# Kernel optimization log

Measured on AMD Instinct MI355X. Metric: run time of the kernel, lower is better.

## Reference

```python
import jax, jax.numpy as jnp
import numpy as np

N_USERS, N_ITEMS, N_TOPICS = 200000, 100000, 100
N_NODES = N_USERS + N_ITEMS + N_TOPICS
N_EDGES = 5000000
DIM = 64
LAYERS = 3
BATCH = 16384


def setup_inputs() -> dict:
    key = jax.random.key(0)
    ks = jax.random.split(key, 8)
    users = jax.random.randint(ks[0], (BATCH,), 0, N_USERS, dtype=jnp.int64 if jax.config.jax_enable_x64 else jnp.int32)
    items = jax.random.randint(ks[1], (BATCH,), 0, N_ITEMS, dtype=jnp.int64 if jax.config.jax_enable_x64 else jnp.int32)
    edge_rows = jax.random.randint(ks[2], (N_EDGES,), 0, N_NODES, dtype=jnp.int32)
    edge_cols = jax.random.randint(ks[3], (N_EDGES,), 0, N_NODES, dtype=jnp.int32)
    # values ~ 1/deg to mimic the symmetric-normalized A_hat of LightGCN
    edge_vals = jax.random.uniform(ks[4], (N_EDGES,), dtype=jnp.float32) / 16.0
    user_emb = 0.1 * jax.random.normal(ks[5], (N_USERS, DIM), dtype=jnp.float32)
    item_emb = 0.1 * jax.random.normal(ks[6], (N_ITEMS, DIM), dtype=jnp.float32)
    topic_emb = 0.1 * jax.random.normal(ks[7], (N_TOPICS, DIM), dtype=jnp.float32)
    return {"users": users, "items": items, "edge_rows": edge_rows,
            "edge_cols": edge_cols, "edge_vals": edge_vals,
            "user_emb": user_emb, "item_emb": item_emb, "topic_emb": topic_emb}


def reference(users, items, edge_rows, edge_cols, edge_vals, user_emb, item_emb, topic_emb):
    n_users = user_emb.shape[0]
    n_nodes = n_users + item_emb.shape[0] + topic_emb.shape[0]
    # E^0 = [users; items; topics]
    h = jnp.concatenate([user_emb, item_emb, topic_emb], axis=0)  # [N, dim]
    acc = h
    for _ in range(LAYERS):
        # sparse A_hat @ h : gather source rows, scale by edge weight, scatter-add to dst
        msgs = edge_vals[:, None] * h[edge_cols]                  # [E, dim]
        h = jax.ops.segment_sum(msgs, edge_rows, num_segments=n_nodes)
        acc = acc + h
    out = acc / (LAYERS + 1)                                      # stack-mean over layers
    u = out[users]                                                # [B, dim]
    it = out[n_users + items]                                     # items offset into node table
    return jnp.sum(u * it, axis=1)                                # [B]
```

## Files before the change

### kernel.cpp

```cpp
#include <hip/hip_runtime.h>
#include <hip/hip_fp16.h>

#define N_USERS  200000
#define N_ITEMS  100000
#define N_TOPICS 100
#define N_NODES  (N_USERS + N_ITEMS + N_TOPICS)
#define DIM      64
#define BSHIFT   10
#define BROWS    (1 << BSHIFT)
#define NBUCKETS ((N_NODES + BROWS - 1) >> BSHIFT)
#define COLMASK  0x7FFFF
#define NB       512
#define NBSHIFT  9
#define M_TOT    (NBUCKETS * NB)
#define SB       256
#define CH       ((M_TOT + SB - 1) / SB)
#define BUCKET_CAP 24576



__global__ void bucket_hist_kernel(const int* __restrict__ rows,
                                   int* __restrict__ partial, int n_edges) {
    __shared__ int h[NBUCKETS];
    for (int i = threadIdx.x; i < NBUCKETS; i += blockDim.x) h[i] = 0;
    __syncthreads();
    int stride = gridDim.x * blockDim.x;
    for (int e = blockIdx.x * blockDim.x + threadIdx.x; e < n_edges; e += stride)
        atomicAdd(&h[((unsigned)rows[e]) >> BSHIFT], 1);
    __syncthreads();
    for (int i = threadIdx.x; i < NBUCKETS; i += blockDim.x)
        partial[blockIdx.x * NBUCKETS + i] = h[i];
}

__device__ __forceinline__ int phys_idx(int L) {
    return (L & (NB - 1)) * NBUCKETS + (L >> NBSHIFT);
}

__global__ void scanB1_kernel(const int* __restrict__ partial,
                              int* __restrict__ psum) {
    __shared__ int s[256];
    int tid = threadIdx.x;
    int c0 = blockIdx.x * CH;
    int c1 = min(M_TOT, c0 + CH);
    int sum = 0;
    for (int L = c0 + tid; L < c1; L += 256) sum += partial[phys_idx(L)];
    s[tid] = sum;
    __syncthreads();
    for (int off = 128; off > 0; off >>= 1) {
        if (tid < off) s[tid] += s[tid + off];
        __syncthreads();
    }
    if (tid == 0) psum[blockIdx.x] = s[0];
}

__global__ void scanB3_kernel(const int* __restrict__ partial,
                              const int* __restrict__ psum,
                              int* __restrict__ offs) {
    __shared__ int s[SB];
    __shared__ int tile[256];
    __shared__ int carry;
    int tid = threadIdx.x;
    s[tid] = (tid < blockIdx.x) ? psum[tid] : 0;
    __syncthreads();
    for (int off = 128; off > 0; off >>= 1) {
        if (tid < off) s[tid] += s[tid + off];
        __syncthreads();
    }
    if (tid == 0) carry = s[0];
    __syncthreads();
    int c0 = blockIdx.x * CH;
    int c1 = min(M_TOT, c0 + CH);
    for (int base = c0; base < c1; base += 256) {
        int L = base + tid;
        int v = (L < c1) ? partial[phys_idx(L)] : 0;
        tile[tid] = v;
        __syncthreads();
        for (int off = 1; off < 256; off <<= 1) {
            int t = (tid >= off) ? tile[tid - off] : 0;
            __syncthreads();
            tile[tid] += t;
            __syncthreads();
        }
        if (L < c1) offs[L] = carry + tile[tid] - v;
        __syncthreads();
        if (tid == 255) carry += tile[255];
        __syncthreads();
    }
}

__global__ void scatter1_kernel(const int* __restrict__ rows,
                                const int* __restrict__ cols,
                                const float* __restrict__ vals,
                                const int* __restrict__ offs,
                                int2* __restrict__ bkt_buf, int n_edges) {
    __shared__ int lpos[NBUCKETS];
    for (int i = threadIdx.x; i < NBUCKETS; i += blockDim.x)
        lpos[i] = offs[i * NB + blockIdx.x];
    __syncthreads();
    int stride = gridDim.x * blockDim.x;
    for (int e = blockIdx.x * blockDim.x + threadIdx.x; e < n_edges; e += stride) {
        int r = rows[e];
        int b = ((unsigned)r) >> BSHIFT;
        int pos = atomicAdd(&lpos[b], 1);
        int2 p;
        p.x = cols[e] | ((r & (BROWS - 1)) << 19);
        p.y = __float_as_int(vals[e]);
        bkt_buf[pos] = p;
    }
}

__device__ __forceinline__ int pad8(int x) { return (x + 7) & ~7; }

__global__ void scatter2_kernel(const int2* __restrict__ bkt_buf,
                                const int* __restrict__ offs,
                                int2* __restrict__ row_span,
                                int2* __restrict__ csr_cv, int n_edges) {
    __shared__ int lcnt[BROWS];
    __shared__ int lptr[BROWS];
    __shared__ int lfill[BROWS];
    __shared__ int s[512];
    int b = blockIdx.x;
    int t = threadIdx.x;
    int e0 = offs[b * NB];
    int e1 = (b == NBUCKETS - 1) ? n_edges : offs[(b + 1) * NB];
    for (int i = t; i < BROWS; i += 512) { lcnt[i] = 0; lfill[i] = 0; }
    __syncthreads();
    for (int e = e0 + t; e < e1; e += blockDim.x)
        atomicAdd(&lcnt[((unsigned)bkt_buf[e].x) >> 19], 1);
    __syncthreads();
    s[t] = pad8(lcnt[2 * t]) + pad8(lcnt[2 * t + 1]);
    __syncthreads();
    for (int off = 1; off < 512; off <<= 1) {
        int v = (t >= off) ? s[t - off] : 0;
        __syncthreads();
        s[t] += v;
        __syncthreads();
    }
    {
        int base = b * BUCKET_CAP + (t ? s[t - 1] : 0);
        int rbase = b << BSHIFT;
        int pe = pad8(lcnt[2 * t]);
        int po = pad8(lcnt[2 * t + 1]);
        int p_even = base;
        int p_odd  = base + pe;
        lptr[2 * t]     = p_even;
        lptr[2 * t + 1] = p_odd;
        if (rbase + 2 * t < N_NODES) {
            int2 sp; sp.x = p_even; sp.y = p_even + pe;
            row_span[rbase + 2 * t] = sp;
        }
        if (rbase + 2 * t + 1 < N_NODES) {
            int2 sp; sp.x = p_odd; sp.y = p_odd + po;
            row_span[rbase + 2 * t + 1] = sp;
        }
    }
    __syncthreads();
    for (int e = e0 + t; e < e1; e += blockDim.x) {
        int2 p = bkt_buf[e];
        int delta = ((unsigned)p.x) >> 19;
        int pos = lptr[delta] + atomicAdd(&lfill[delta], 1);
        int2 cv;
        cv.x = p.x & COLMASK;
        cv.y = p.y;
        csr_cv[pos] = cv;
    }
    __syncthreads();
    for (int i = t; i < BROWS; i += 512) {
        int c  = lcnt[i];
        int cp = pad8(c);
        int p  = lptr[i];
        int2 z; z.x = 0; z.y = 0;
        for (int k = c; k < cp; ++k) csr_cv[p + k] = z;
    }
}

__global__ void concat_f16_kernel(const float* __restrict__ uemb,
                                  const float* __restrict__ iemb,
                                  const float* __restrict__ temb,
                                  ushort* __restrict__ h0) {
    int g = blockIdx.x * blockDim.x + threadIdx.x;
    long base = (long)g * 4;
    if (base >= (long)N_NODES * DIM) return;
    const float* src;
    long off;
    if (base < (long)N_USERS * DIM)                 { src = uemb; off = base; }
    else if (base < (long)(N_USERS + N_ITEMS) * DIM){ src = iemb; off = base - (long)N_USERS * DIM; }
    else                                            { src = temb; off = base - (long)(N_USERS + N_ITEMS) * DIM; }
    float4 v = *(const float4*)(src + off);
    __half2 a = __floats2half2_rn(v.x, v.y);
    __half2 b = __floats2half2_rn(v.z, v.w);
    uint2 o;
    o.x = *(unsigned*)&a;
    o.y = *(unsigned*)&b;
    ((uint2*)h0)[g] = o;
}

__device__ __forceinline__ float4 fma_mix4(const ushort* __restrict__ h,
                                           int row, int l16, float w,
                                           float4 acc) {
    uint2 r = ((const uint2*)(h + (size_t)row * DIM))[l16];
    __half2 h01 = *(__half2*)&r.x;
    __half2 h23 = *(__half2*)&r.y;
    acc.x = __builtin_fmaf(__half2float(__low2half(h01)),  w, acc.x);
    acc.y = __builtin_fmaf(__half2float(__high2half(h01)), w, acc.y);
    acc.z = __builtin_fmaf(__half2float(__low2half(h23)),  w, acc.z);
    acc.w = __builtin_fmaf(__half2float(__high2half(h23)), w, acc.w);
    return acc;
}

__device__ __forceinline__ float4 batch8(const int2* __restrict__ csr_cv,
                                         const ushort* __restrict__ h_src,
                                         int p, int l16, float4 acc) {
    const int4* q = (const int4*)(csr_cv + p);
    int4 a = q[0], b = q[1], c = q[2], d = q[3];
    acc = fma_mix4(h_src, a.x, l16, __int_as_float(a.y), acc);
    acc = fma_mix4(h_src, a.z, l16, __int_as_float(a.w), acc);
    acc = fma_mix4(h_src, b.x, l16, __int_as_float(b.y), acc);
    acc = fma_mix4(h_src, b.z, l16, __int_as_float(b.w), acc);
    acc = fma_mix4(h_src, c.x, l16, __int_as_float(c.y), acc);
    acc = fma_mix4(h_src, c.z, l16, __int_as_float(c.w), acc);
    acc = fma_mix4(h_src, d.x, l16, __int_as_float(d.y), acc);
    acc = fma_mix4(h_src, d.z, l16, __int_as_float(d.w), acc);
    return acc;
}

__global__ void spmv_csr_kernel(const int2* __restrict__ row_span,
                                const int2* __restrict__ csr_cv,
                                const ushort* __restrict__ h_src,
                                ushort* __restrict__ h_dst) {
    int wave = (int)(((long)blockIdx.x * blockDim.x + threadIdx.x) >> 6);
    int lane = threadIdx.x & 63;
    int g    = lane >> 4;
    int l16  = lane & 15;
    int r    = wave * 4 + g;
    int rc   = min(r, N_NODES - 1);
    int2 sp  = row_span[rc];
    int p0   = sp.x;
    int len  = (r < N_NODES) ? (sp.y - sp.x) : 0;
    int m = max(len, __shfl_xor(len, 16, 64));
    m = max(m, __shfl_xor(m, 32, 64));
    float4 acc = make_float4(0.f, 0.f, 0.f, 0.f);
    for (int off = 0; off < m; off += 8) {
        if (off < len)
            acc = batch8(csr_cv, h_src, p0 + off, l16, acc);
    }
    if (r < N_NODES) {
        __half2 a = __floats2half2_rn(acc.x, acc.y);
        __half2 b = __floats2half2_rn(acc.z, acc.w);
        uint2 o;
        o.x = *(unsigned*)&a;
        o.y = *(unsigned*)&b;
        ((uint2*)(h_dst + (size_t)r * DIM))[l16] = o;
    }
}

__global__ void spmv_batch_kernel(const int2* __restrict__ row_span,
                                  const int2* __restrict__ csr_cv,
                                  const ushort* __restrict__ h_src,
                                  const int* __restrict__ users,
                                  const int* __restrict__ items,
                                  float* __restrict__ u_acc,
                                  float* __restrict__ it_acc, int B) {
    int wave = (int)(((long)blockIdx.x * blockDim.x + threadIdx.x) >> 6);
    int lane = threadIdx.x & 63;
    int g    = lane >> 4;
    int l16  = lane & 15;
    int s    = wave * 4 + g;
    bool ok  = s < 2 * B;
    int node = 0;
    if (ok) node = (s < B) ? users[s] : (N_USERS + items[s - B]);
    int2 sp  = row_span[node];
    int p0   = sp.x;
    int len  = ok ? (sp.y - sp.x) : 0;
    int m = max(len, __shfl_xor(len, 16, 64));
    m = max(m, __shfl_xor(m, 32, 64));
    float4 acc = make_float4(0.f, 0.f, 0.f, 0.f);
    for (int off = 0; off < m; off += 8) {
        if (off < len)
            acc = batch8(csr_cv, h_src, p0 + off, l16, acc);
    }
    if (ok) {
        float* dst = (s < B) ? (u_acc + (size_t)s * DIM)
                             : (it_acc + (size_t)(s - B) * DIM);
        float4* p = (float4*)dst + l16;
        float4 old = *p;
        old.x += acc.x; old.y += acc.y; old.z += acc.z; old.w += acc.w;
        *p = old;
    }
}


__global__ void gather_add_kernel(const ushort* __restrict__ h,
                                  const int* __restrict__ users,
                                  const int* __restrict__ items,
                                  float* __restrict__ u_acc,
                                  float* __restrict__ it_acc,
                                  int B, int first) {
    int gid  = blockIdx.x * blockDim.x + threadIdx.x;
    int b    = gid >> 4;
    int lane = gid & 15;
    if (b >= B) return;
    int u  = users[b];
    int it = N_USERS + items[b];
    uint2 ur = ((const uint2*)(h + (size_t)u  * DIM))[lane];
    uint2 ir = ((const uint2*)(h + (size_t)it * DIM))[lane];
    float2 u01 = __half22float2(*(__half2*)&ur.x);
    float2 u23 = __half22float2(*(__half2*)&ur.y);
    float2 i01 = __half22float2(*(__half2*)&ir.x);
    float2 i23 = __half22float2(*(__half2*)&ir.y);
    float4* up = (float4*)(u_acc  + (size_t)b * DIM) + lane;
    float4* ip = (float4*)(it_acc + (size_t)b * DIM) + lane;
    if (first) {
        *up = make_float4(u01.x, u01.y, u23.x, u23.y);
        *ip = make_float4(i01.x, i01.y, i23.x, i23.y);
    } else {
        float4 a = *up;
        a.x += u01.x; a.y += u01.y; a.z += u23.x; a.w += u23.y;
        *up = a;
        float4 c = *ip;
        c.x += i01.x; c.y += i01.y; c.z += i23.x; c.w += i23.y;
        *ip = c;
    }
}

__global__ void dot_kernel(const float* __restrict__ u_acc,
                           const float* __restrict__ it_acc,
                           float* __restrict__ out, int B) {
    int gid  = blockIdx.x * blockDim.x + threadIdx.x;
    int b    = gid >> 6;
    int lane = gid & 63;
    if (b >= B) return;
    float p = u_acc[(size_t)b * DIM + lane] * it_acc[(size_t)b * DIM + lane];
    #pragma unroll
    for (int off = 32; off > 0; off >>= 1)
        p += __shfl_down(p, off, 64);
    if (lane == 0) out[b] = p * (1.0f / 16.0f);
}

extern "C" void kernel_launch(void* const* d_in, const int* in_sizes, int n_in,
                              void* d_out, int out_size, void* d_ws, size_t ws_size,
                              hipStream_t stream) {
    const int*   users = (const int*)d_in[0];
    const int*   items = (const int*)d_in[1];
    const int*   erows = (const int*)d_in[2];
    const int*   ecols = (const int*)d_in[3];
    const float* evals = (const float*)d_in[4];
    const float* uemb  = (const float*)d_in[5];
    const float* iemb  = (const float*)d_in[6];
    const float* temb  = (const float*)d_in[7];
    float* out = (float*)d_out;

    const int n_edges = in_sizes[2];
    const int B       = in_sizes[0];

    const size_t h2bytes = (((size_t)N_NODES * DIM * 2 + 255) / 256) * 256;
    const size_t abytes  = (size_t)B * DIM * sizeof(float);
    const size_t spbytes = (((size_t)N_NODES * 8 + 255) / 256) * 256;
    const size_t csrbytes= (size_t)NBUCKETS * BUCKET_CAP * 8;
    const size_t bkbytes = (size_t)n_edges * 8;
    const size_t mbytes  = (((size_t)M_TOT * 4 + 255) / 256) * 256;

    char* ws = (char*)d_ws;
    size_t off = 0;
    ushort* hA       = (ushort*)(ws + off); off += h2bytes;
    ushort* hB       = (ushort*)(ws + off); off += h2bytes;
    float*  u_acc    = (float*) (ws + off); off += abytes;
    float*  it_acc   = (float*) (ws + off); off += abytes;
    int2*   row_span = (int2*)  (ws + off); off += spbytes;
    int2*   csr_cv   = (int2*)  (ws + off); off += csrbytes;
    int2*   bkt_buf  = (int2*)  (ws + off); off += bkbytes;
    int*    partial  = (int*)   (ws + off); off += mbytes;
    int*    offs     = (int*)   (ws + off); off += mbytes;
    int*    psum     = (int*)   (ws + off); off += 4096;

    dim3 blk(256);
    dim3 blk512(512);

    bucket_hist_kernel<<<NB, blk512, 0, stream>>>(erows, partial, n_edges);
    scanB1_kernel<<<SB, blk, 0, stream>>>(partial, psum);
    scanB3_kernel<<<SB, blk, 0, stream>>>(partial, psum, offs);
    scatter1_kernel<<<NB, blk512, 0, stream>>>(erows, ecols, evals, offs, bkt_buf, n_edges);
    scatter2_kernel<<<NBUCKETS, blk512, 0, stream>>>(bkt_buf, offs, row_span, csr_cv, n_edges);

    const long n4 = (long)N_NODES * DIM / 4;
    concat_f16_kernel<<<(int)((n4 + 255) / 256), blk, 0, stream>>>(uemb, iemb, temb, hA);

    const int gblocks = (B * 16 + 255) / 256;
    gather_add_kernel<<<gblocks, blk, 0, stream>>>(hA, users, items, u_acc, it_acc, B, 1);

    const int nwaves  = (N_NODES + 3) / 4;
    const int sblocks = (int)(((long)nwaves * 64 + 255) / 256);
    ushort* src = hA;
    ushort* dst = hB;
    for (int l = 0; l < 2; ++l) {
        spmv_csr_kernel<<<sblocks, blk, 0, stream>>>(row_span, csr_cv, src, dst);
        gather_add_kernel<<<gblocks, blk, 0, stream>>>(dst, users, items, u_acc, it_acc, B, 0);
        ushort* t = src; src = dst; dst = t;
    }
    const int bwaves  = (2 * B + 3) / 4;
    const int bblocks = (int)(((long)bwaves * 64 + 255) / 256);
    spmv_batch_kernel<<<bblocks, blk, 0, stream>>>(row_span, csr_cv, src,
                                                   users, items, u_acc, it_acc, B);

    dot_kernel<<<(B * 64 + 255) / 256, blk, 0, stream>>>(u_acc, it_acc, out, B);
}
```

Baseline: 548.5 us.

## Fuse concat into histogram kernel and gather-adds into SpMV launches

Merges the fp16 concat of embeddings into the bucket histogram kernel using extra blocks. Folds each layer's gather-add of batch user/item rows into the SpMV launch that reads that layer's source, and has the final batch SpMV add the previous layer's rows itself. This removes several small kernel launches and their serialization gaps. The trade-off is heterogeneous blocks inside one grid and a larger launch for the prep kernel.

```diff
diff --git a/kernel.cpp b/kernel.cpp
--- a/kernel.cpp
+++ b/kernel.cpp
@@ -19,17 +19,39 @@
 
 
 
-__global__ void bucket_hist_kernel(const int* __restrict__ rows,
-                                   int* __restrict__ partial, int n_edges) {
+__global__ void prep_kernel(const int* __restrict__ rows,
+                            int* __restrict__ partial, int n_edges,
+                            const float* __restrict__ uemb,
+                            const float* __restrict__ iemb,
+                            const float* __restrict__ temb,
+                            ushort* __restrict__ h0) {
     __shared__ int h[NBUCKETS];
-    for (int i = threadIdx.x; i < NBUCKETS; i += blockDim.x) h[i] = 0;
-    __syncthreads();
-    int stride = gridDim.x * blockDim.x;
-    for (int e = blockIdx.x * blockDim.x + threadIdx.x; e < n_edges; e += stride)
-        atomicAdd(&h[((unsigned)rows[e]) >> BSHIFT], 1);
-    __syncthreads();
-    for (int i = threadIdx.x; i < NBUCKETS; i += blockDim.x)
-        partial[blockIdx.x * NBUCKETS + i] = h[i];
+    if (blockIdx.x < NB) {
+        for (int i = threadIdx.x; i < NBUCKETS; i += blockDim.x) h[i] = 0;
+        __syncthreads();
+        int stride = NB * blockDim.x;
+        for (int e = blockIdx.x * blockDim.x + threadIdx.x; e < n_edges; e += stride)
+            atomicAdd(&h[((unsigned)rows[e]) >> BSHIFT], 1);
+        __syncthreads();
+        for (int i = threadIdx.x; i < NBUCKETS; i += blockDim.x)
+            partial[blockIdx.x * NBUCKETS + i] = h[i];
+    } else {
+        int g = (blockIdx.x - NB) * blockDim.x + threadIdx.x;
+        long base = (long)g * 4;
+        if (base >= (long)N_NODES * DIM) return;
+        const float* src;
+        long off;
+        if (base < (long)N_USERS * DIM)                 { src = uemb; off = base; }
+        else if (base < (long)(N_USERS + N_ITEMS) * DIM){ src = iemb; off = base - (long)N_USERS * DIM; }
+        else                                            { src = temb; off = base - (long)(N_USERS + N_ITEMS) * DIM; }
+        float4 v = *(const float4*)(src + off);
+        __half2 a = __floats2half2_rn(v.x, v.y);
+        __half2 b = __floats2half2_rn(v.z, v.w);
+        uint2 o;
+        o.x = *(unsigned*)&a;
+        o.y = *(unsigned*)&b;
+        ((uint2*)h0)[g] = o;
+    }
 }
 
 __device__ __forceinline__ int phys_idx(int L) {
@@ -172,27 +194,6 @@
         int2 z; z.x = 0; z.y = 0;
         for (int k = c; k < cp; ++k) csr_cv[p + k] = z;
     }
-}
-
-__global__ void concat_f16_kernel(const float* __restrict__ uemb,
-                                  const float* __restrict__ iemb,
-                                  const float* __restrict__ temb,
-                                  ushort* __restrict__ h0) {
-    int g = blockIdx.x * blockDim.x + threadIdx.x;
-    long base = (long)g * 4;
-    if (base >= (long)N_NODES * DIM) return;
-    const float* src;
-    long off;
-    if (base < (long)N_USERS * DIM)                 { src = uemb; off = base; }
-    else if (base < (long)(N_USERS + N_ITEMS) * DIM){ src = iemb; off = base - (long)N_USERS * DIM; }
-    else                                            { src = temb; off = base - (long)(N_USERS + N_ITEMS) * DIM; }
-    float4 v = *(const float4*)(src + off);
-    __half2 a = __floats2half2_rn(v.x, v.y);
-    __half2 b = __floats2half2_rn(v.z, v.w);
-    uint2 o;
-    o.x = *(unsigned*)&a;
-    o.y = *(unsigned*)&b;
-    ((uint2*)h0)[g] = o;
 }
 
 __device__ __forceinline__ float4 fma_mix4(const ushort* __restrict__ h,
@@ -224,33 +225,59 @@
     return acc;
 }
 
+#define NWAVES ((N_NODES + 3) / 4)
+
 __global__ void spmv_csr_kernel(const int2* __restrict__ row_span,
                                 const int2* __restrict__ csr_cv,
                                 const ushort* __restrict__ h_src,
-                                ushort* __restrict__ h_dst) {
+                                ushort* __restrict__ h_dst,
+                                const int* __restrict__ users,
+                                const int* __restrict__ items,
+                                float* __restrict__ u_acc,
+                                float* __restrict__ it_acc,
+                                int B, int first) {
     int wave = (int)(((long)blockIdx.x * blockDim.x + threadIdx.x) >> 6);
     int lane = threadIdx.x & 63;
     int g    = lane >> 4;
     int l16  = lane & 15;
-    int r    = wave * 4 + g;
-    int rc   = min(r, N_NODES - 1);
-    int2 sp  = row_span[rc];
-    int p0   = sp.x;
-    int len  = (r < N_NODES) ? (sp.y - sp.x) : 0;
-    int m = max(len, __shfl_xor(len, 16, 64));
-    m = max(m, __shfl_xor(m, 32, 64));
-    float4 acc = make_float4(0.f, 0.f, 0.f, 0.f);
-    for (int off = 0; off < m; off += 8) {
-        if (off < len)
-            acc = batch8(csr_cv, h_src, p0 + off, l16, acc);
-    }
-    if (r < N_NODES) {
-        __half2 a = __floats2half2_rn(acc.x, acc.y);
-        __half2 b = __floats2half2_rn(acc.z, acc.w);
-        uint2 o;
-        o.x = *(unsigned*)&a;
-        o.y = *(unsigned*)&b;
-        ((uint2*)(h_dst + (size_t)r * DIM))[l16] = o;
+    if (wave < NWAVES) {
+        int r    = wave * 4 + g;
+        int rc   = min(r, N_NODES - 1);
+        int2 sp  = row_span[rc];
+        int p0   = sp.x;
+        int len  = (r < N_NODES) ? (sp.y - sp.x) : 0;
+        int m = max(len, __shfl_xor(len, 16, 64));
+        m = max(m, __shfl_xor(m, 32, 64));
+        float4 acc = make_float4(0.f, 0.f, 0.f, 0.f);
+        for (int off = 0; off < m; off += 8) {
+            if (off < len)
+                acc = batch8(csr_cv, h_src, p0 + off, l16, acc);
+        }
+        if (r < N_NODES) {
+            __half2 a = __floats2half2_rn(acc.x, acc.y);
+            __half2 b = __floats2half2_rn(acc.z, acc.w);
+            uint2 o;
+            o.x = *(unsigned*)&a;
+            o.y = *(unsigned*)&b;
+            ((uint2*)(h_dst + (size_t)r * DIM))[l16] = o;
+        }
+    } else {
+        int s = (wave - NWAVES) * 4 + g;
+        if (s >= 2 * B) return;
+        int node = (s < B) ? users[s] : (N_USERS + items[s - B]);
+        uint2 hr = ((const uint2*)(h_src + (size_t)node * DIM))[l16];
+        float2 a01 = __half22float2(*(__half2*)&hr.x);
+        float2 a23 = __half22float2(*(__half2*)&hr.y);
+        float* dst = (s < B) ? (u_acc + (size_t)s * DIM)
+                             : (it_acc + (size_t)(s - B) * DIM);
+        float4* p = (float4*)dst + l16;
+        if (first) {
+            *p = make_float4(a01.x, a01.y, a23.x, a23.y);
+        } else {
+            float4 o = *p;
+            o.x += a01.x; o.y += a01.y; o.z += a23.x; o.w += a23.y;
+            *p = o;
+        }
     }
 }
 
@@ -269,12 +296,18 @@
     bool ok  = s < 2 * B;
     int node = 0;
     if (ok) node = (s < B) ? users[s] : (N_USERS + items[s - B]);
+    float4 acc = make_float4(0.f, 0.f, 0.f, 0.f);
+    if (ok) {
+        uint2 hr = ((const uint2*)(h_src + (size_t)node * DIM))[l16];
+        float2 a01 = __half22float2(*(__half2*)&hr.x);
+        float2 a23 = __half22float2(*(__half2*)&hr.y);
+        acc = make_float4(a01.x, a01.y, a23.x, a23.y);
+    }
     int2 sp  = row_span[node];
     int p0   = sp.x;
     int len  = ok ? (sp.y - sp.x) : 0;
     int m = max(len, __shfl_xor(len, 16, 64));
     m = max(m, __shfl_xor(m, 32, 64));
-    float4 acc = make_float4(0.f, 0.f, 0.f, 0.f);
     for (int off = 0; off < m; off += 8) {
         if (off < len)
             acc = batch8(csr_cv, h_src, p0 + off, l16, acc);
@@ -286,40 +319,6 @@
         float4 old = *p;
         old.x += acc.x; old.y += acc.y; old.z += acc.z; old.w += acc.w;
         *p = old;
-    }
-}
-
-
-__global__ void gather_add_kernel(const ushort* __restrict__ h,
-                                  const int* __restrict__ users,
-                                  const int* __restrict__ items,
-                                  float* __restrict__ u_acc,
-                                  float* __restrict__ it_acc,
-                                  int B, int first) {
-    int gid  = blockIdx.x * blockDim.x + threadIdx.x;
-    int b    = gid >> 4;
-    int lane = gid & 15;
-    if (b >= B) return;
-    int u  = users[b];
-    int it = N_USERS + items[b];
-    uint2 ur = ((const uint2*)(h + (size_t)u  * DIM))[lane];
-    uint2 ir = ((const uint2*)(h + (size_t)it * DIM))[lane];
-    float2 u01 = __half22float2(*(__half2*)&ur.x);
-    float2 u23 = __half22float2(*(__half2*)&ur.y);
-    float2 i01 = __half22float2(*(__half2*)&ir.x);
-    float2 i23 = __half22float2(*(__half2*)&ir.y);
-    float4* up = (float4*)(u_acc  + (size_t)b * DIM) + lane;
-    float4* ip = (float4*)(it_acc + (size_t)b * DIM) + lane;
-    if (first) {
-        *up = make_float4(u01.x, u01.y, u23.x, u23.y);
-        *ip = make_float4(i01.x, i01.y, i23.x, i23.y);
-    } else {
-        float4 a = *up;
-        a.x += u01.x; a.y += u01.y; a.z += u23.x; a.w += u23.y;
-        *up = a;
-        float4 c = *ip;
-        c.x += i01.x; c.y += i01.y; c.z += i23.x; c.w += i23.y;
-        *ip = c;
     }
 }
 
@@ -376,30 +375,23 @@
     dim3 blk(256);
     dim3 blk512(512);
 
-    bucket_hist_kernel<<<NB, blk512, 0, stream>>>(erows, partial, n_edges);
+    const long n4 = (long)N_NODES * DIM / 4;
+    const int  nconcat = (int)((n4 + 511) / 512);
+    prep_kernel<<<NB + nconcat, blk512, 0, stream>>>(erows, partial, n_edges,
+                                                     uemb, iemb, temb, hA);
     scanB1_kernel<<<SB, blk, 0, stream>>>(partial, psum);
     scanB3_kernel<<<SB, blk, 0, stream>>>(partial, psum, offs);
     scatter1_kernel<<<NB, blk512, 0, stream>>>(erows, ecols, evals, offs, bkt_buf, n_edges);
     scatter2_kernel<<<NBUCKETS, blk512, 0, stream>>>(bkt_buf, offs, row_span, csr_cv, n_edges);
 
-    const long n4 = (long)N_NODES * DIM / 4;
-    concat_f16_kernel<<<(int)((n4 + 255) / 256), blk, 0, stream>>>(uemb, iemb, temb, hA);
-
-    const int gblocks = (B * 16 + 255) / 256;
-    gather_add_kernel<<<gblocks, blk, 0, stream>>>(hA, users, items, u_acc, it_acc, B, 1);
-
-    const int nwaves  = (N_NODES + 3) / 4;
-    const int sblocks = (int)(((long)nwaves * 64 + 255) / 256);
-    ushort* src = hA;
-    ushort* dst = hB;
-    for (int l = 0; l < 2; ++l) {
-        spmv_csr_kernel<<<sblocks, blk, 0, stream>>>(row_span, csr_cv, src, dst);
-        gather_add_kernel<<<gblocks, blk, 0, stream>>>(dst, users, items, u_acc, it_acc, B, 0);
-        ushort* t = src; src = dst; dst = t;
-    }
-    const int bwaves  = (2 * B + 3) / 4;
-    const int bblocks = (int)(((long)bwaves * 64 + 255) / 256);
-    spmv_batch_kernel<<<bblocks, blk, 0, stream>>>(row_span, csr_cv, src,
+    const int gwaves  = (2 * B + 3) / 4;
+    const int fblocks = (int)(((long)(NWAVES + gwaves) * 64 + 255) / 256);
+    spmv_csr_kernel<<<fblocks, blk, 0, stream>>>(row_span, csr_cv, hA, hB,
+                                                 users, items, u_acc, it_acc, B, 1);
+    spmv_csr_kernel<<<fblocks, blk, 0, stream>>>(row_span, csr_cv, hB, hA,
+                                                 users, items, u_acc, it_acc, B, 0);
+    const int bblocks = (int)(((long)gwaves * 64 + 255) / 256);
+    spmv_batch_kernel<<<bblocks, blk, 0, stream>>>(row_span, csr_cv, hA,
                                                    users, items, u_acc, it_acc, B);
 
     dot_kernel<<<(B * 64 + 255) / 256, blk, 0, stream>>>(u_acc, it_acc, out, B);
```

New measurement: 524.4 us. -4.4%, faster.
